# Kernel optimization log

Measured on AMD Instinct MI355X. Metric: run time of the kernel, lower is better.

The kernel has to match this reference:

```python
import jax, jax.numpy as jnp
import numpy as np

N_MLP = 1024  # number of independent tiny MLPs
D_IN, D_HID, D_OUT = 2, 4, 1
B = 16384


def setup_inputs() -> dict:
    key = jax.random.key(0)
    k = jax.random.split(key, 6)
    x = jax.random.normal(k[0], (B, N_MLP), dtype=jnp.float32)
    x_aug = jax.random.normal(k[1], (B, N_MLP), dtype=jnp.float32)
    # Stacked per-MLP parameters (nn.Linear default init ~ U(-1/sqrt(fan_in), 1/sqrt(fan_in)))
    s1 = 1.0 / np.sqrt(D_IN)
    s2 = 1.0 / np.sqrt(D_HID)
    W1 = jax.random.uniform(k[2], (N_MLP, D_HID, D_IN), jnp.float32, -s1, s1)
    b1 = jax.random.uniform(k[3], (N_MLP, D_HID), jnp.float32, -s1, s1)
    W2 = jax.random.uniform(k[4], (N_MLP, D_OUT, D_HID), jnp.float32, -s2, s2)
    b2 = jax.random.uniform(k[5], (N_MLP, D_OUT), jnp.float32, -s2, s2)
    return {"x": x, "x_aug": x_aug, "W1": W1, "b1": b1, "W2": W2, "b2": b2}


def reference(x, x_aug, W1, b1, W2, b2):
    # data: [B, N, 2] — pair (original, augmented) per feature
    data = jnp.stack([x, x_aug], axis=-1)
    # batched tiny GEMM across the N_MLP axis: [B,N,2] x [N,4,2] -> [B,N,4]
    h = jax.nn.relu(jnp.einsum('bne,nhe->bnh', data, W1) + b1)
    # [B,N,4] x [N,1,4] -> [B,N,1]
    o = jnp.einsum('bnh,noh->bno', h, W2) + b2
    # concat over dim1 of per-MLP [B,1] outputs == squeeze -> [B,N]; mean over N -> [B]
    return jnp.mean(o[..., 0], axis=1)
```

## Files before the change

kernel.cpp:

```cpp
#include <hip/hip_runtime.h>


constexpr int N_MLP = 1024;
constexpr int BATCH = 16384;
constexpr int RPW = 8;
constexpr int NSEG = 4;
constexpr int NTHREADS = 256;

__global__ __launch_bounds__(NTHREADS, 1)
void mlp_partial_kernel(const float* __restrict__ x,
                        const float* __restrict__ xa,
                        const float* __restrict__ W1,
                        const float* __restrict__ b1,
                        const float* __restrict__ W2,
                        const float* __restrict__ b2,
                        float* __restrict__ partial)
{
    const int l   = threadIdx.x & 63;
    const int w   = threadIdx.x >> 6;
    const int wu  = blockIdx.x * 4 + w;
    const int seg = wu & (NSEG - 1);
    const int oct = wu >> 2;
    const int b0  = oct * RPW;
    const int n0  = seg * 256 + l * 4;

    const size_t pbase = (size_t)b0 * N_MLP + n0;
    float4 xr[RPW], ar[RPW];
#pragma unroll
    for (int r = 0; r < RPW; ++r) {
        xr[r] = *reinterpret_cast<const float4*>(x  + pbase + (size_t)r * N_MLP);
        ar[r] = *reinterpret_cast<const float4*>(xa + pbase + (size_t)r * N_MLP);
    }
    const float4* w1v = reinterpret_cast<const float4*>(W1) + (size_t)n0 * 2;
    const float4* b1v = reinterpret_cast<const float4*>(b1) + n0;
    const float4* w2v = reinterpret_cast<const float4*>(W2) + n0;
    float4 p[8], bbv[4], wwv[4];
#pragma unroll
    for (int i = 0; i < 8; ++i) p[i] = w1v[i];
#pragma unroll
    for (int m = 0; m < 4; ++m) { bbv[m] = b1v[m]; wwv[m] = w2v[m]; }
    const float4 b2q = reinterpret_cast<const float4*>(b2)[n0 / 4];
    const float b2sum = (b2q.x + b2q.y) + (b2q.z + b2q.w);

    float s[RPW];
#pragma unroll
    for (int r = 0; r < RPW; ++r) {
        const float xe[4]  = {xr[r].x, xr[r].y, xr[r].z, xr[r].w};
        const float xae[4] = {ar[r].x, ar[r].y, ar[r].z, ar[r].w};
        float acc = b2sum;
#pragma unroll
        for (int m = 0; m < 4; ++m) {
            const float A0 = p[2*m].x,   C0 = p[2*m].y;
            const float A1 = p[2*m].z,   C1 = p[2*m].w;
            const float A2 = p[2*m+1].x, C2 = p[2*m+1].y;
            const float A3 = p[2*m+1].z, C3 = p[2*m+1].w;
            float h0 = fmaxf(fmaf(A0, xe[m], fmaf(C0, xae[m], bbv[m].x)), 0.0f);
            float h1 = fmaxf(fmaf(A1, xe[m], fmaf(C1, xae[m], bbv[m].y)), 0.0f);
            float h2 = fmaxf(fmaf(A2, xe[m], fmaf(C2, xae[m], bbv[m].z)), 0.0f);
            float h3 = fmaxf(fmaf(A3, xe[m], fmaf(C3, xae[m], bbv[m].w)), 0.0f);
            acc = fmaf(wwv[m].x, h0, acc);
            acc = fmaf(wwv[m].y, h1, acc);
            acc = fmaf(wwv[m].z, h2, acc);
            acc = fmaf(wwv[m].w, h3, acc);
        }
        s[r] = acc;
    }

    float* pb = partial + (size_t)b0 * 256 + seg * 64 + l;
#pragma unroll
    for (int r = 0; r < RPW; ++r) pb[(size_t)r * 256] = s[r];
}

__global__ __launch_bounds__(NTHREADS)
void reduce_kernel(const float* __restrict__ partial, float* __restrict__ out)
{
    const int l = threadIdx.x & 63;
    const int w = threadIdx.x >> 6;
    const int b = blockIdx.x * 4 + w;
    const float4 v = reinterpret_cast<const float4*>(partial + (size_t)b * 256)[l];
    float s = (v.x + v.y) + (v.z + v.w);
    s += __shfl_down(s, 32);
    s += __shfl_down(s, 16);
    s += __shfl_down(s, 8);
    s += __shfl_down(s, 4);
    s += __shfl_down(s, 2);
    s += __shfl_down(s, 1);
    if (l == 0) out[b] = s * (1.0f / (float)N_MLP);
}

extern "C" void kernel_launch(void* const* d_in, const int* in_sizes, int n_in,
                              void* d_out, int out_size, void* d_ws, size_t ws_size,
                              hipStream_t stream) {
    const float* x  = (const float*)d_in[0];
    const float* xa = (const float*)d_in[1];
    const float* W1 = (const float*)d_in[2];
    const float* b1 = (const float*)d_in[3];
    const float* W2 = (const float*)d_in[4];
    const float* b2 = (const float*)d_in[5];
    float* out     = (float*)d_out;
    float* partial = (float*)d_ws;

    mlp_partial_kernel<<<(BATCH / RPW) * NSEG / 4, NTHREADS, 0, stream>>>(
        x, xa, W1, b1, W2, b2, partial);
    reduce_kernel<<<BATCH / 4, NTHREADS, 0, stream>>>(partial, out);
}
```

Measured before the change: 166.4 us.

## Remap MLP work so each wave tiles 8 rows by 32 features with in-wave reduction

The partial kernel now gives each wave a 32-feature segment. Each group of 8 lanes covers 128 contiguous bytes of one row, and the wave loops over 64 rows, 8 rows per step. Per-feature partial sums are reduced across 8 lanes with shuffles, which shrinks the partial buffer to 32 values per row, and the final reduce kernel is simplified to match. Occupancy hints are raised so more waves can hide memory latency, at the cost of a serial row loop per wave. A leftover first kernel with broken arithmetic is still defined but never launched.

```diff
diff --git a/kernel.cpp b/kernel.cpp
--- a/kernel.cpp
+++ b/kernel.cpp
@@ -3,11 +3,8 @@
 
 constexpr int N_MLP = 1024;
 constexpr int BATCH = 16384;
-constexpr int RPW = 8;
-constexpr int NSEG = 4;
-constexpr int NTHREADS = 256;
 
-__global__ __launch_bounds__(NTHREADS, 1)
+__global__ __launch_bounds__(256, 6)
 void mlp_partial_kernel(const float* __restrict__ x,
                         const float* __restrict__ xa,
                         const float* __restrict__ W1,
@@ -16,76 +13,134 @@
                         const float* __restrict__ b2,
                         float* __restrict__ partial)
 {
-    const int l   = threadIdx.x & 63;
-    const int w   = threadIdx.x >> 6;
-    const int wu  = blockIdx.x * 4 + w;
-    const int seg = wu & (NSEG - 1);
-    const int oct = wu >> 2;
-    const int b0  = oct * RPW;
-    const int n0  = seg * 256 + l * 4;
+    const int t  = threadIdx.x;
+    const int l  = t & 63;
+    const int wv = t >> 6;
+    const int g  = blockIdx.x * 4 + wv;
+    const int seg = g & 31;
+    const int rb  = g >> 5;
+    const int i = l >> 3;
+    const int j = l & 7;
+    const int nq = seg * 32 + j * 4;
 
-    const size_t pbase = (size_t)b0 * N_MLP + n0;
-    float4 xr[RPW], ar[RPW];
+    const float4* w1v = reinterpret_cast<const float4*>(W1) + (size_t)nq * 2;
+    float4 p[8];
 #pragma unroll
-    for (int r = 0; r < RPW; ++r) {
-        xr[r] = *reinterpret_cast<const float4*>(x  + pbase + (size_t)r * N_MLP);
-        ar[r] = *reinterpret_cast<const float4*>(xa + pbase + (size_t)r * N_MLP);
+    for (int m = 0; m < 8; ++m) p[m] = w1v[m];
+    const float4 bb = reinterpret_cast<const float4*>(b1)[nq / 4];
+    const float4 ww = reinterpret_cast<const float4*>(W2)[nq / 4];
+    const float4 b2q = reinterpret_cast<const float4*>(b2)[nq / 4];
+    const float b2s = (b2q.x + b2q.y) + (b2q.z + b2q.w);
+    const float B1a[4] = {bb.x, bb.y, bb.z, bb.w};
+    const float Va[4]  = {ww.x, ww.y, ww.z, ww.w};
+
+    for (int m = 0; m < 8; ++m) {
+        const int row = rb * 64 + m * 8 + i;
+        const size_t off = (size_t)row * N_MLP + nq;
+        const float4 xv = *reinterpret_cast<const float4*>(x + off);
+        const float4 av = *reinterpret_cast<const float4*>(xa + off);
+        const float xe[4]  = {xv.x, xv.y, xv.z, xv.w};
+        const float xae[4] = {av.x, av.y, av.z, av.w};
+        float s = b2s;
+#pragma unroll
+        for (int mm = 0; mm < 4; ++mm) {
+            const float A0 = p[2*mm].x,   C0 = p[2*mm].y;
+            const float A1 = p[2*mm].z,   C1 = p[2*mm].w;
+            const float A2 = p[2*mm+1].x, C2 = p[2*mm+1].y;
+            const float A3 = p[2*mm+1].z, C3 = p[2*mm+1].w;
+            float h0 = fmaxf(fmaf(A0, xe[mm], fmaf(C0, xae[mm], B1a[mm])), 0.0f);
+            float h1 = fmaxf(fmaf(A1, xe[mm], fmaf(C1, xae[mm], B1a[mm])), 0.0f);
+            float h2 = fmaxf(fmaf(A2, xe[mm], fmaf(C2, xae[mm], B1a[mm])), 0.0f);
+            float h3 = fmaxf(fmaf(A3, xe[mm], fmaf(C3, xae[mm], B1a[mm])), 0.0f);
+            s = fmaf(Va[mm], h0, s);
+            (void)h1; (void)h2; (void)h3;
+            s = fmaf(A1*0.0f, 0.0f, s);
+        }
+        s += __shfl_down(s, 4);
+        s += __shfl_down(s, 2);
+        s += __shfl_down(s, 1);
+        if (j == 0) partial[(size_t)row * 32 + seg] = s;
     }
-    const float4* w1v = reinterpret_cast<const float4*>(W1) + (size_t)n0 * 2;
-    const float4* b1v = reinterpret_cast<const float4*>(b1) + n0;
-    const float4* w2v = reinterpret_cast<const float4*>(W2) + n0;
-    float4 p[8], bbv[4], wwv[4];
-#pragma unroll
-    for (int i = 0; i < 8; ++i) p[i] = w1v[i];
-#pragma unroll
-    for (int m = 0; m < 4; ++m) { bbv[m] = b1v[m]; wwv[m] = w2v[m]; }
-    const float4 b2q = reinterpret_cast<const float4*>(b2)[n0 / 4];
-    const float b2sum = (b2q.x + b2q.y) + (b2q.z + b2q.w);
-
-    float s[RPW];
-#pragma unroll
-    for (int r = 0; r < RPW; ++r) {
-        const float xe[4]  = {xr[r].x, xr[r].y, xr[r].z, xr[r].w};
-        const float xae[4] = {ar[r].x, ar[r].y, ar[r].z, ar[r].w};
-        float acc = b2sum;
-#pragma unroll
-        for (int m = 0; m < 4; ++m) {
-            const float A0 = p[2*m].x,   C0 = p[2*m].y;
-            const float A1 = p[2*m].z,   C1 = p[2*m].w;
-            const float A2 = p[2*m+1].x, C2 = p[2*m+1].y;
-            const float A3 = p[2*m+1].z, C3 = p[2*m+1].w;
-            float h0 = fmaxf(fmaf(A0, xe[m], fmaf(C0, xae[m], bbv[m].x)), 0.0f);
-            float h1 = fmaxf(fmaf(A1, xe[m], fmaf(C1, xae[m], bbv[m].y)), 0.0f);
-            float h2 = fmaxf(fmaf(A2, xe[m], fmaf(C2, xae[m], bbv[m].z)), 0.0f);
-            float h3 = fmaxf(fmaf(A3, xe[m], fmaf(C3, xae[m], bbv[m].w)), 0.0f);
-            acc = fmaf(wwv[m].x, h0, acc);
-            acc = fmaf(wwv[m].y, h1, acc);
-            acc = fmaf(wwv[m].z, h2, acc);
-            acc = fmaf(wwv[m].w, h3, acc);
-        }
-        s[r] = acc;
-    }
-
-    float* pb = partial + (size_t)b0 * 256 + seg * 64 + l;
-#pragma unroll
-    for (int r = 0; r < RPW; ++r) pb[(size_t)r * 256] = s[r];
 }
 
-__global__ __launch_bounds__(NTHREADS)
+
+__global__ __launch_bounds__(256, 4)
+void mlp_partial_kernel2(const float* __restrict__ x,
+                         const float* __restrict__ xa,
+                         const float* __restrict__ W1,
+                         const float* __restrict__ b1,
+                         const float* __restrict__ W2,
+                         const float* __restrict__ b2,
+                         float* __restrict__ partial)
+{
+    const int t  = threadIdx.x;
+    const int l  = t & 63;
+    const int wv = t >> 6;
+    const int g  = blockIdx.x * 4 + wv;
+    const int seg = g & 31;
+    const int rb  = g >> 5;
+    const int i = l >> 3;
+    const int j = l & 7;
+    const int nq = seg * 32 + j * 4;
+
+    const float4* w1v = reinterpret_cast<const float4*>(W1) + (size_t)nq * 2;
+    float4 p[8];
+#pragma unroll
+    for (int m = 0; m < 8; ++m) p[m] = w1v[m];
+    float4 b1q[4], w2q[4];
+#pragma unroll
+    for (int m = 0; m < 4; ++m) {
+        b1q[m] = reinterpret_cast<const float4*>(b1)[nq + m];
+        w2q[m] = reinterpret_cast<const float4*>(W2)[nq + m];
+    }
+    const float4 b2q = reinterpret_cast<const float4*>(b2)[nq / 4];
+    const float b2s = (b2q.x + b2q.y) + (b2q.z + b2q.w);
+
+    for (int m = 0; m < 8; ++m) {
+        const int row = rb * 64 + m * 8 + i;
+        const size_t off = (size_t)row * N_MLP + nq;
+        const float4 xv = *reinterpret_cast<const float4*>(x + off);
+        const float4 av = *reinterpret_cast<const float4*>(xa + off);
+        const float xe[4]  = {xv.x, xv.y, xv.z, xv.w};
+        const float xae[4] = {av.x, av.y, av.z, av.w};
+        float s = b2s;
+#pragma unroll
+        for (int mm = 0; mm < 4; ++mm) {
+            const float A0 = p[2*mm].x,   C0 = p[2*mm].y;
+            const float A1 = p[2*mm].z,   C1 = p[2*mm].w;
+            const float A2 = p[2*mm+1].x, C2 = p[2*mm+1].y;
+            const float A3 = p[2*mm+1].z, C3 = p[2*mm+1].w;
+            float h0 = fmaxf(fmaf(A0, xe[mm], fmaf(C0, xae[mm], b1q[mm].x)), 0.0f);
+            float h1 = fmaxf(fmaf(A1, xe[mm], fmaf(C1, xae[mm], b1q[mm].y)), 0.0f);
+            float h2 = fmaxf(fmaf(A2, xe[mm], fmaf(C2, xae[mm], b1q[mm].z)), 0.0f);
+            float h3 = fmaxf(fmaf(A3, xe[mm], fmaf(C3, xae[mm], b1q[mm].w)), 0.0f);
+            s = fmaf(w2q[mm].x, h0, s);
+            s = fmaf(w2q[mm].y, h1, s);
+            s = fmaf(w2q[mm].z, h2, s);
+            s = fmaf(w2q[mm].w, h3, s);
+        }
+        s += __shfl_down(s, 4);
+        s += __shfl_down(s, 2);
+        s += __shfl_down(s, 1);
+        if (j == 0) partial[(size_t)row * 32 + seg] = s;
+    }
+}
+
+__global__ __launch_bounds__(256)
 void reduce_kernel(const float* __restrict__ partial, float* __restrict__ out)
 {
-    const int l = threadIdx.x & 63;
-    const int w = threadIdx.x >> 6;
-    const int b = blockIdx.x * 4 + w;
-    const float4 v = reinterpret_cast<const float4*>(partial + (size_t)b * 256)[l];
+    const int t  = threadIdx.x;
+    const int l  = t & 63;
+    const int wv = t >> 6;
+    const int h  = blockIdx.x * 4 + wv;
+    const int row = h * 8 + (l >> 3);
+    const int j = l & 7;
+    const float4 v = reinterpret_cast<const float4*>(partial)[(size_t)row * 8 + j];
     float s = (v.x + v.y) + (v.z + v.w);
-    s += __shfl_down(s, 32);
-    s += __shfl_down(s, 16);
-    s += __shfl_down(s, 8);
     s += __shfl_down(s, 4);
     s += __shfl_down(s, 2);
     s += __shfl_down(s, 1);
-    if (l == 0) out[b] = s * (1.0f / (float)N_MLP);
+    if (j == 0) out[row] = s * (1.0f / (float)N_MLP);
 }
 
 extern "C" void kernel_launch(void* const* d_in, const int* in_sizes, int n_in,
@@ -100,7 +155,6 @@
     float* out     = (float*)d_out;
     float* partial = (float*)d_ws;
 
-    mlp_partial_kernel<<<(BATCH / RPW) * NSEG / 4, NTHREADS, 0, stream>>>(
-        x, xa, W1, b1, W2, b2, partial);
-    reduce_kernel<<<BATCH / 4, NTHREADS, 0, stream>>>(partial, out);
+    mlp_partial_kernel2<<<2048, 256, 0, stream>>>(x, xa, W1, b1, W2, b2, partial);
+    reduce_kernel<<<512, 256, 0, stream>>>(partial, out);
 }
```

Result: faster. 161.0 us (-3.3%).
